# Optimization experiments

Hardware: AMD Instinct MI355X
Metric: run time of the kernel (lower is better)

The kernel has to match this reference:

```python
import jax, jax.numpy as jnp
import numpy as np

N_BLOCKS = 4
DIN = 4000      # features per input block
DE = 128        # embed dims per block
DLAT = 512      # latent dim per block
ALPHA = 0.3     # Keras LeakyReLU default negative slope


def setup_inputs() -> dict:
    key = jax.random.key(0)
    ks = jax.random.split(key, 7)
    N = 4096
    x = jax.random.normal(ks[0], (N, N_BLOCKS * DIN), dtype=jnp.float32)
    mask = jax.random.bernoulli(ks[1], 0.5, (N, N_BLOCKS * DIN))
    embed = jax.random.normal(ks[2], (N, N_BLOCKS * DE), dtype=jnp.float32)
    batches = jax.random.normal(ks[3], (N, 8), dtype=jnp.float32)
    mean_vals = jax.random.normal(ks[4], (N_BLOCKS * DIN,), dtype=jnp.float32)
    fan_in = DIN + DE + 8
    W = jax.random.normal(ks[5], (N_BLOCKS, fan_in, DLAT), dtype=jnp.float32) / np.sqrt(fan_in)
    b = jnp.zeros((N_BLOCKS, DLAT), dtype=jnp.float32)
    return {"x": x, "mask": mask, "embed": embed, "batches": batches,
            "mean_vals": mean_vals, "W": W, "b": b}


def reference(x, mask, embed, batches, mean_vals, W, b):
    N = x.shape[0]
    db = batches.shape[1]
    # masked mean-centering: x = where(mask, x - mean, 0)
    xm = jnp.where(mask, x - mean_vals[None, :], jnp.zeros((), x.dtype))
    # equal-sized splits == reshape into [N, B, din] / [N, B, de]
    xb = xm.reshape(N, N_BLOCKS, DIN)
    eb = embed.reshape(N, N_BLOCKS, DE)
    bb = jnp.broadcast_to(batches[:, None, :], (N, N_BLOCKS, db))
    inp = jnp.concatenate([xb, eb, bb], axis=-1)  # [N, B, DIN+DE+db]
    h = jnp.einsum('nbi,bio->nbo', inp, W) + b[None, :, :]  # grouped GEMM
    h = jnp.where(h >= 0, h, ALPHA * h)  # LeakyReLU(alpha=0.3)
    return h.reshape(N, N_BLOCKS * DLAT)  # concat of per-block outputs
```

## Files before the change

kernel.cpp:

```cpp
#include <hip/hip_runtime.h>

#define NROWS 4096
#define NBLK 4
#define DIN 4000
#define DE 128
#define DB 8
#define DLAT 512
#define FANIN 4136
#define KPAD 4224
#define NKT 66
#define XC 16000
#define OUTC 2048
#define TC 192

typedef __attribute__((ext_vector_type(8))) short short8;
typedef __attribute__((ext_vector_type(4))) float floatx4;

__device__ __forceinline__ unsigned short f2bf(float f) {
    unsigned int u = __builtin_bit_cast(unsigned int, f);
    u = (u + 0x7FFFu + ((u >> 16) & 1u)) >> 16;
    return (unsigned short)u;
}

__device__ __forceinline__ void async16(const void* g, void* l) {
    __builtin_amdgcn_global_load_lds(
        (const __attribute__((address_space(1))) void*)g,
        (__attribute__((address_space(3))) void*)l, 16, 0, 0);
}

__global__ void prep_w(const float* __restrict__ W, unsigned short* __restrict__ Wp) {
    __shared__ unsigned short tile[64 * 68];
    int bid = blockIdx.x;
    int nt = bid & 7;
    int t2 = bid >> 3;
    int kt = t2 % 66;
    int b  = t2 / 66;
    int tid = threadIdx.x;
    int n0 = nt * 64;
    int k0 = kt * 64;
#pragma unroll
    for (int i = 0; i < 4; ++i) {
        int c = i * 256 + tid;
        int r = c >> 4;
        int q = (c & 15) * 4;
        int pk = k0 + r;
        int wr = (pk < DIN) ? pk : ((pk >= 4032 && pk < 4168) ? pk - 32 : -1);
        float4 v = make_float4(0.f, 0.f, 0.f, 0.f);
        if (wr >= 0)
            v = *reinterpret_cast<const float4*>(W + ((size_t)b * FANIN + wr) * DLAT + n0 + q);
        ushort4 u4 = make_ushort4(f2bf(v.x), f2bf(v.y), f2bf(v.z), f2bf(v.w));
        *reinterpret_cast<ushort4*>(&tile[r * 68 + q]) = u4;
    }
    __syncthreads();
#pragma unroll
    for (int i = 0; i < 2; ++i) {
        int c = i * 256 + tid;
        int nl = c >> 3;
        int kc = c & 7;
        unsigned short o[8];
#pragma unroll
        for (int j = 0; j < 8; ++j) o[j] = tile[(kc * 8 + j) * 68 + nl];
        *reinterpret_cast<short8*>(Wp + ((size_t)(b * DLAT + n0 + nl)) * KPAD + k0 + kc * 8) =
            *reinterpret_cast<const short8*>(o);
    }
}

__global__ void prep_x(const float* __restrict__ x, const int* __restrict__ mask,
                       const float* __restrict__ mean, const float* __restrict__ embed,
                       const float* __restrict__ batches, unsigned short* __restrict__ Xp) {
    int c = blockIdx.x * 256 + threadIdx.x;
    int chunk = c % 528;
    int rb    = c / 528;
    int b   = rb & 3;
    int row = rb >> 2;
    int k   = chunk * 8;
    short8 v8 = (short8){0, 0, 0, 0, 0, 0, 0, 0};
    if (k < DIN) {
        size_t gi = (size_t)row * XC + b * DIN + k;
        const float4* xp = reinterpret_cast<const float4*>(x + gi);
        const int4*   mp = reinterpret_cast<const int4*>(mask + gi);
        const float4* ep = reinterpret_cast<const float4*>(mean + b * DIN + k);
        float4 x0 = xp[0], x1 = xp[1];
        int4   m0 = mp[0], m1 = mp[1];
        float4 e0 = ep[0], e1 = ep[1];
        float f0 = m0.x ? x0.x - e0.x : 0.f;
        float f1 = m0.y ? x0.y - e0.y : 0.f;
        float f2 = m0.z ? x0.z - e0.z : 0.f;
        float f3 = m0.w ? x0.w - e0.w : 0.f;
        float f4 = m1.x ? x1.x - e1.x : 0.f;
        float f5 = m1.y ? x1.y - e1.y : 0.f;
        float f6 = m1.z ? x1.z - e1.z : 0.f;
        float f7 = m1.w ? x1.w - e1.w : 0.f;
        v8 = (short8){(short)f2bf(f0), (short)f2bf(f1), (short)f2bf(f2), (short)f2bf(f3),
                      (short)f2bf(f4), (short)f2bf(f5), (short)f2bf(f6), (short)f2bf(f7)};
    } else if (k >= 4032 && k < 4160) {
        const float4* ep = reinterpret_cast<const float4*>(
            embed + (size_t)row * (NBLK * DE) + b * DE + (k - 4032));
        float4 a = ep[0], bb = ep[1];
        v8 = (short8){(short)f2bf(a.x), (short)f2bf(a.y), (short)f2bf(a.z), (short)f2bf(a.w),
                      (short)f2bf(bb.x), (short)f2bf(bb.y), (short)f2bf(bb.z), (short)f2bf(bb.w)};
    } else if (k == 4160) {
        const float4* bp = reinterpret_cast<const float4*>(batches + (size_t)row * DB);
        float4 a = bp[0], bb = bp[1];
        v8 = (short8){(short)f2bf(a.x), (short)f2bf(a.y), (short)f2bf(a.z), (short)f2bf(a.w),
                      (short)f2bf(bb.x), (short)f2bf(bb.y), (short)f2bf(bb.z), (short)f2bf(bb.w)};
    }
    *reinterpret_cast<short8*>(Xp + (size_t)rb * KPAD + k) = v8;
}

__global__ __launch_bounds__(256, 3) void gemm_x(
    const float* __restrict__ bias, const unsigned short* __restrict__ Wp,
    const unsigned short* __restrict__ Xp, float* __restrict__ out) {
    __shared__ unsigned short Asm_[128 * 64];
    __shared__ unsigned short Bsm_[128 * 64];

    int bid = blockIdx.x;
    int nt  = bid & 3;
    int b   = (bid >> 2) & 3;
    int mt  = bid >> 4;
    int tid  = threadIdx.x;
    int lane = tid & 63;
    int w    = tid >> 6;
    int wm   = w >> 1;
    int wn   = w & 1;
    int quad = lane >> 4;
    int l16  = lane & 15;
    int row0 = mt * 128;
    int n0   = nt * 128;

    floatx4 acc[4][4];
#pragma unroll
    for (int m = 0; m < 4; ++m)
#pragma unroll
        for (int n = 0; n < 4; ++n) acc[m][n] = (floatx4){0.f, 0.f, 0.f, 0.f};

    const unsigned short* Abase = Xp + ((size_t)row0 * NBLK + b) * KPAD;
    const unsigned short* Bbase = Wp + ((size_t)(b * DLAT + n0)) * KPAD;

    for (int kt = 0; kt < NKT; ++kt) {
        int k0 = kt * 64;
#pragma unroll
        for (int i = 0; i < 4; ++i) {
            int c  = i * 256 + tid;
            int r  = c >> 3;
            int cg = (c & 7) ^ (r & 7);
            async16(Abase + (size_t)r * (NBLK * KPAD) + k0 + cg * 8, &Asm_[c * 8]);
        }
#pragma unroll
        for (int i = 0; i < 4; ++i) {
            int c  = i * 256 + tid;
            int nl = c >> 3;
            int cg = (c & 7) ^ (nl & 7);
            async16(Bbase + (size_t)nl * KPAD + k0 + cg * 8, &Bsm_[c * 8]);
        }
        __syncthreads();
#pragma unroll
        for (int s = 0; s < 2; ++s) {
            short8 af[4], bfr[4];
#pragma unroll
            for (int m = 0; m < 4; ++m) {
                int ar = wm * 64 + m * 16 + l16;
                af[m] = *reinterpret_cast<const short8*>(
                    &Asm_[ar * 64 + (((s * 4 + quad) ^ (ar & 7)) * 8)]);
            }
#pragma unroll
            for (int n = 0; n < 4; ++n) {
                int br = wn * 64 + n * 16 + l16;
                bfr[n] = *reinterpret_cast<const short8*>(
                    &Bsm_[br * 64 + (((s * 4 + quad) ^ (br & 7)) * 8)]);
            }
#pragma unroll
            for (int m = 0; m < 4; ++m)
#pragma unroll
                for (int n = 0; n < 4; ++n)
                    acc[m][n] = __builtin_amdgcn_mfma_f32_16x16x32_bf16(
                        af[m], bfr[n], acc[m][n], 0, 0, 0);
        }
        __syncthreads();
    }

#pragma unroll
    for (int m = 0; m < 4; ++m) {
#pragma unroll
        for (int n = 0; n < 4; ++n) {
            int col_l = wn * 64 + n * 16 + l16;
            float bv = bias[b * DLAT + n0 + col_l];
#pragma unroll
            for (int r = 0; r < 4; ++r) {
                int row_l = wm * 64 + m * 16 + quad * 4 + r;
                float v = acc[m][n][r] + bv;
                v = v >= 0.f ? v : 0.3f * v;
                out[(size_t)(row0 + row_l) * OUTC + b * DLAT + n0 + col_l] = v;
            }
        }
    }
}

__global__ void prep_t(const float* __restrict__ embed, const float* __restrict__ batches,
                       unsigned short* __restrict__ T) {
    int i  = blockIdx.x * 256 + threadIdx.x;
    int t  = i % TC;
    int nb = i / TC;
    int b  = nb & 3;
    int n  = nb >> 2;
    float v = 0.f;
    if (t < DE)            v = embed[(size_t)n * (NBLK * DE) + b * DE + t];
    else if (t < DE + DB)  v = batches[(size_t)n * DB + (t - DE)];
    T[i] = f2bf(v);
}

__global__ __launch_bounds__(256, 3) void gemm_k(
    const float* __restrict__ x, const int* __restrict__ mask,
    const float* __restrict__ mean, const float* __restrict__ bias,
    const unsigned short* __restrict__ Wp, const unsigned short* __restrict__ T,
    float* __restrict__ out) {
    __shared__ unsigned short Asm_[128 * 64];
    __shared__ unsigned short Bsm_[128 * 64];

    int bid = blockIdx.x;
    int nt  = bid & 3;
    int b   = (bid >> 2) & 3;
    int mt  = bid >> 4;
    int tid  = threadIdx.x;
    int lane = tid & 63;
    int w    = tid >> 6;
    int wm   = w >> 1;
    int wn   = w & 1;
    int quad = lane >> 4;
    int l16  = lane & 15;
    int row0 = mt * 128;
    int n0   = nt * 128;

    floatx4 acc[4][4];
#pragma unroll
    for (int m = 0; m < 4; ++m)
#pragma unroll
        for (int n = 0; n < 4; ++n) acc[m][n] = (floatx4){0.f, 0.f, 0.f, 0.f};

    for (int kt = 0; kt < NKT; ++kt) {
        if (kt < 63) {
#pragma unroll
            for (int i = 0; i < 4; ++i) {
                int c  = i * 256 + tid;
                int r  = c >> 3;
                int cg = c & 7;
                int col = kt * 64 + cg * 8;
                short8 v8 = (short8){0, 0, 0, 0, 0, 0, 0, 0};
                if (col < DIN) {
                    size_t gi = (size_t)(row0 + r) * XC + (size_t)b * DIN + col;
                    const float4* xp = reinterpret_cast<const float4*>(x + gi);
                    const int4*   mp = reinterpret_cast<const int4*>(mask + gi);
                    const float4* ep = reinterpret_cast<const float4*>(mean + b * DIN + col);
                    float4 x0 = xp[0], x1 = xp[1];
                    int4   m0 = mp[0], m1 = mp[1];
                    float4 e0 = ep[0], e1 = ep[1];
                    float f0 = m0.x ? x0.x - e0.x : 0.f;
                    float f1 = m0.y ? x0.y - e0.y : 0.f;
                    float f2 = m0.z ? x0.z - e0.z : 0.f;
                    float f3 = m0.w ? x0.w - e0.w : 0.f;
                    float f4 = m1.x ? x1.x - e1.x : 0.f;
                    float f5 = m1.y ? x1.y - e1.y : 0.f;
                    float f6 = m1.z ? x1.z - e1.z : 0.f;
                    float f7 = m1.w ? x1.w - e1.w : 0.f;
                    v8 = (short8){(short)f2bf(f0), (short)f2bf(f1), (short)f2bf(f2),
                                  (short)f2bf(f3), (short)f2bf(f4), (short)f2bf(f5),
                                  (short)f2bf(f6), (short)f2bf(f7)};
                }
                *reinterpret_cast<short8*>(&Asm_[r * 64 + ((cg ^ (r & 7)) * 8)]) = v8;
            }
        } else {
#pragma unroll
            for (int i = 0; i < 4; ++i) {
                int c  = i * 256 + tid;
                int r  = c >> 3;
                int cg = (c & 7) ^ (r & 7);
                async16(T + ((size_t)(row0 + r) * NBLK + b) * TC + (kt - 63) * 64 + cg * 8,
                        &Asm_[c * 8]);
            }
        }
#pragma unroll
        for (int i = 0; i < 4; ++i) {
            int c  = i * 256 + tid;
            int nl = c >> 3;
            int cg = (c & 7) ^ (nl & 7);
            async16(Wp + ((size_t)(b * DLAT + n0 + nl)) * KPAD + kt * 64 + cg * 8,
                    &Bsm_[c * 8]);
        }
        __syncthreads();
#pragma unroll
        for (int s = 0; s < 2; ++s) {
            short8 af[4], bfr[4];
#pragma unroll
            for (int m = 0; m < 4; ++m) {
                int ar = wm * 64 + m * 16 + l16;
                af[m] = *reinterpret_cast<const short8*>(
                    &Asm_[ar * 64 + (((s * 4 + quad) ^ (ar & 7)) * 8)]);
            }
#pragma unroll
            for (int n = 0; n < 4; ++n) {
                int br = wn * 64 + n * 16 + l16;
                bfr[n] = *reinterpret_cast<const short8*>(
                    &Bsm_[br * 64 + (((s * 4 + quad) ^ (br & 7)) * 8)]);
            }
#pragma unroll
            for (int m = 0; m < 4; ++m)
#pragma unroll
                for (int n = 0; n < 4; ++n)
                    acc[m][n] = __builtin_amdgcn_mfma_f32_16x16x32_bf16(
                        af[m], bfr[n], acc[m][n], 0, 0, 0);
        }
        __syncthreads();
    }

#pragma unroll
    for (int m = 0; m < 4; ++m) {
#pragma unroll
        for (int n = 0; n < 4; ++n) {
            int col_l = wn * 64 + n * 16 + l16;
            float bv = bias[b * DLAT + n0 + col_l];
#pragma unroll
            for (int r = 0; r < 4; ++r) {
                int row_l = wm * 64 + m * 16 + quad * 4 + r;
                float v = acc[m][n][r] + bv;
                v = v >= 0.f ? v : 0.3f * v;
                out[(size_t)(row0 + row_l) * OUTC + b * DLAT + n0 + col_l] = v;
            }
        }
    }
}

extern "C" void kernel_launch(void* const* d_in, const int* in_sizes, int n_in,
                              void* d_out, int out_size, void* d_ws, size_t ws_size,
                              hipStream_t stream) {
    const float* x       = (const float*)d_in[0];
    const int*   mask    = (const int*)d_in[1];
    const float* embed   = (const float*)d_in[2];
    const float* batches = (const float*)d_in[3];
    const float* mean    = (const float*)d_in[4];
    const float* W       = (const float*)d_in[5];
    const float* bias    = (const float*)d_in[6];
    float* out = (float*)d_out;

    unsigned short* Wp = (unsigned short*)d_ws;
    size_t wp_elems = (size_t)NBLK * DLAT * KPAD;
    size_t xp_elems = (size_t)NROWS * NBLK * KPAD;
    size_t need_fast = (wp_elems + xp_elems) * 2;

    prep_w<<<dim3(2112), dim3(256), 0, stream>>>(W, Wp);

    if (ws_size >= need_fast) {
        unsigned short* Xp = Wp + wp_elems;
        prep_x<<<dim3(33792), dim3(256), 0, stream>>>(x, mask, mean, embed, batches, Xp);
        gemm_x<<<dim3(512), dim3(256), 0, stream>>>(bias, Wp, Xp, out);
    } else {
        unsigned short* T = Wp + wp_elems;
        prep_t<<<dim3(12288), dim3(256), 0, stream>>>(embed, batches, T);
        gemm_k<<<dim3(512), dim3(256), 0, stream>>>(x, mask, mean, bias, Wp, T, out);
    }
}
```

Before: 649.5 us.

## Fuse masked input preparation into a double-buffered grouped GEMM kernel

Drops the separate prep_x pass that wrote a bf16 copy of the centered inputs to workspace. The new gemm_f kernel reads x, mask, mean, embed and batches directly, applies the mask and mean subtraction, converts to bf16 in registers and writes the result to LDS. Global loads for the next k-tile are prefetched into registers and asynchronous LDS copies while the current tile runs on the MFMA units, using double-buffered LDS. Each block now covers 64 rows by the full 512 outputs of one block group with 512 threads. This removes a large intermediate write and re-read, but uses about 144KB of LDS per block, so only one block fits per CU and latency hiding rests on the prefetch.

```diff
diff --git a/kernel.cpp b/kernel.cpp
--- a/kernel.cpp
+++ b/kernel.cpp
@@ -13,8 +13,12 @@
 #define OUTC 2048
 #define TC 192
 
+#define PW_GRID 2112
+
 typedef __attribute__((ext_vector_type(8))) short short8;
 typedef __attribute__((ext_vector_type(4))) float floatx4;
+typedef float __attribute__((ext_vector_type(4))) f32x4;
+typedef int   __attribute__((ext_vector_type(4))) i32x4;
 
 __device__ __forceinline__ unsigned short f2bf(float f) {
     unsigned int u = __builtin_bit_cast(unsigned int, f);
@@ -65,68 +69,27 @@
     }
 }
 
-__global__ void prep_x(const float* __restrict__ x, const int* __restrict__ mask,
-                       const float* __restrict__ mean, const float* __restrict__ embed,
-                       const float* __restrict__ batches, unsigned short* __restrict__ Xp) {
-    int c = blockIdx.x * 256 + threadIdx.x;
-    int chunk = c % 528;
-    int rb    = c / 528;
-    int b   = rb & 3;
-    int row = rb >> 2;
-    int k   = chunk * 8;
-    short8 v8 = (short8){0, 0, 0, 0, 0, 0, 0, 0};
-    if (k < DIN) {
-        size_t gi = (size_t)row * XC + b * DIN + k;
-        const float4* xp = reinterpret_cast<const float4*>(x + gi);
-        const int4*   mp = reinterpret_cast<const int4*>(mask + gi);
-        const float4* ep = reinterpret_cast<const float4*>(mean + b * DIN + k);
-        float4 x0 = xp[0], x1 = xp[1];
-        int4   m0 = mp[0], m1 = mp[1];
-        float4 e0 = ep[0], e1 = ep[1];
-        float f0 = m0.x ? x0.x - e0.x : 0.f;
-        float f1 = m0.y ? x0.y - e0.y : 0.f;
-        float f2 = m0.z ? x0.z - e0.z : 0.f;
-        float f3 = m0.w ? x0.w - e0.w : 0.f;
-        float f4 = m1.x ? x1.x - e1.x : 0.f;
-        float f5 = m1.y ? x1.y - e1.y : 0.f;
-        float f6 = m1.z ? x1.z - e1.z : 0.f;
-        float f7 = m1.w ? x1.w - e1.w : 0.f;
-        v8 = (short8){(short)f2bf(f0), (short)f2bf(f1), (short)f2bf(f2), (short)f2bf(f3),
-                      (short)f2bf(f4), (short)f2bf(f5), (short)f2bf(f6), (short)f2bf(f7)};
-    } else if (k >= 4032 && k < 4160) {
-        const float4* ep = reinterpret_cast<const float4*>(
-            embed + (size_t)row * (NBLK * DE) + b * DE + (k - 4032));
-        float4 a = ep[0], bb = ep[1];
-        v8 = (short8){(short)f2bf(a.x), (short)f2bf(a.y), (short)f2bf(a.z), (short)f2bf(a.w),
-                      (short)f2bf(bb.x), (short)f2bf(bb.y), (short)f2bf(bb.z), (short)f2bf(bb.w)};
-    } else if (k == 4160) {
-        const float4* bp = reinterpret_cast<const float4*>(batches + (size_t)row * DB);
-        float4 a = bp[0], bb = bp[1];
-        v8 = (short8){(short)f2bf(a.x), (short)f2bf(a.y), (short)f2bf(a.z), (short)f2bf(a.w),
-                      (short)f2bf(bb.x), (short)f2bf(bb.y), (short)f2bf(bb.z), (short)f2bf(bb.w)};
-    }
-    *reinterpret_cast<short8*>(Xp + (size_t)rb * KPAD + k) = v8;
-}
-
-__global__ __launch_bounds__(256, 3) void gemm_x(
-    const float* __restrict__ bias, const unsigned short* __restrict__ Wp,
-    const unsigned short* __restrict__ Xp, float* __restrict__ out) {
-    __shared__ unsigned short Asm_[128 * 64];
-    __shared__ unsigned short Bsm_[128 * 64];
+__global__ __launch_bounds__(512, 2) void gemm_f(
+    const float* __restrict__ x, const int* __restrict__ mask,
+    const float* __restrict__ mean, const float* __restrict__ embed,
+    const float* __restrict__ batches, const float* __restrict__ bias,
+    const unsigned short* __restrict__ Wp, float* __restrict__ out) {
+    __shared__ unsigned short Asm_[2][64 * 64];
+    __shared__ unsigned short Bsm_[2][512 * 64];
 
     int bid = blockIdx.x;
-    int nt  = bid & 3;
-    int b   = (bid >> 2) & 3;
-    int mt  = bid >> 4;
+    int b   = bid & 3;
+    int mt  = bid >> 2;
+    int row0 = mt * 64;
     int tid  = threadIdx.x;
     int lane = tid & 63;
     int w    = tid >> 6;
-    int wm   = w >> 1;
-    int wn   = w & 1;
     int quad = lane >> 4;
     int l16  = lane & 15;
-    int row0 = mt * 128;
-    int n0   = nt * 128;
+    int r    = tid >> 3;
+    int cgl  = tid & 7;
+
+    const unsigned short* Bbase = Wp + (size_t)b * DLAT * KPAD;
 
     floatx4 acc[4][4];
 #pragma unroll
@@ -134,66 +97,133 @@
 #pragma unroll
         for (int n = 0; n < 4; ++n) acc[m][n] = (floatx4){0.f, 0.f, 0.f, 0.f};
 
-    const unsigned short* Abase = Xp + ((size_t)row0 * NBLK + b) * KPAD;
-    const unsigned short* Bbase = Wp + ((size_t)(b * DLAT + n0)) * KPAD;
-
+    f32x4 xa, xb, ea, eb;
+    i32x4 mka, mkb;
+    int amode;
+
+#define STAGE_B(NB, KT) do {                                                   \
+    int k0_ = (KT) * 64;                                                       \
+    _Pragma("unroll")                                                          \
+    for (int i_ = 0; i_ < 8; ++i_) {                                           \
+        int c_  = i_ * 512 + tid;                                              \
+        int nl_ = c_ >> 3;                                                     \
+        int cg_ = (c_ & 7) ^ (nl_ & 7);                                        \
+        async16(Bbase + (size_t)nl_ * KPAD + k0_ + cg_ * 8,                    \
+                &Bsm_[NB][c_ * 8]);                                            \
+    }                                                                          \
+} while (0)
+
+#define LOAD_A(KT) do {                                                        \
+    int col_ = (KT) * 64 + cgl * 8;                                            \
+    amode = 3;                                                                 \
+    if (col_ < DIN) {                                                          \
+        amode = 0;                                                             \
+        size_t gi_ = (size_t)(row0 + r) * XC + (size_t)b * DIN + col_;         \
+        const f32x4* xp_ = reinterpret_cast<const f32x4*>(x + gi_);            \
+        const i32x4* mp_ = reinterpret_cast<const i32x4*>(mask + gi_);         \
+        xa  = __builtin_nontemporal_load(xp_);                                 \
+        xb  = __builtin_nontemporal_load(xp_ + 1);                             \
+        mka = __builtin_nontemporal_load(mp_);                                 \
+        mkb = __builtin_nontemporal_load(mp_ + 1);                             \
+        const f32x4* ep_ = reinterpret_cast<const f32x4*>(mean + b * DIN + col_); \
+        ea = ep_[0]; eb = ep_[1];                                              \
+    } else if (col_ >= 4032 && col_ < 4160) {                                  \
+        amode = 1;                                                             \
+        const f32x4* ep_ = reinterpret_cast<const f32x4*>(                     \
+            embed + (size_t)(row0 + r) * (NBLK * DE) + b * DE + (col_ - 4032)); \
+        ea = ep_[0]; eb = ep_[1];                                              \
+    } else if (col_ == 4160) {                                                 \
+        amode = 1;                                                             \
+        const f32x4* bp_ = reinterpret_cast<const f32x4*>(                     \
+            batches + (size_t)(row0 + r) * DB);                                \
+        ea = bp_[0]; eb = bp_[1];                                              \
+    }                                                                          \
+} while (0)
+
+#define WRITE_A(NB) do {                                                       \
+    short8 v8_ = (short8){0, 0, 0, 0, 0, 0, 0, 0};                             \
+    if (amode == 0) {                                                          \
+        float f0_ = mka.x ? xa.x - ea.x : 0.f;                                 \
+        float f1_ = mka.y ? xa.y - ea.y : 0.f;                                 \
+        float f2_ = mka.z ? xa.z - ea.z : 0.f;                                 \
+        float f3_ = mka.w ? xa.w - ea.w : 0.f;                                 \
+        float f4_ = mkb.x ? xb.x - eb.x : 0.f;                                 \
+        float f5_ = mkb.y ? xb.y - eb.y : 0.f;                                 \
+        float f6_ = mkb.z ? xb.z - eb.z : 0.f;                                 \
+        float f7_ = mkb.w ? xb.w - eb.w : 0.f;                                 \
+        v8_ = (short8){(short)f2bf(f0_), (short)f2bf(f1_), (short)f2bf(f2_),   \
+                       (short)f2bf(f3_), (short)f2bf(f4_), (short)f2bf(f5_),   \
+                       (short)f2bf(f6_), (short)f2bf(f7_)};                    \
+    } else if (amode == 1) {                                                   \
+        v8_ = (short8){(short)f2bf(ea.x), (short)f2bf(ea.y), (short)f2bf(ea.z),\
+                       (short)f2bf(ea.w), (short)f2bf(eb.x), (short)f2bf(eb.y),\
+                       (short)f2bf(eb.z), (short)f2bf(eb.w)};                  \
+    }                                                                          \
+    *reinterpret_cast<short8*>(&Asm_[NB][r * 64 + ((cgl ^ (r & 7)) * 8)]) = v8_; \
+} while (0)
+
+#define COMPUTE(BUF) do {                                                      \
+    _Pragma("unroll")                                                          \
+    for (int s_ = 0; s_ < 2; ++s_) {                                           \
+        short8 af_[4], bf_[4];                                                 \
+        _Pragma("unroll")                                                      \
+        for (int m_ = 0; m_ < 4; ++m_) {                                       \
+            int ar_ = m_ * 16 + l16;                                           \
+            af_[m_] = *reinterpret_cast<const short8*>(                        \
+                &Asm_[BUF][ar_ * 64 + (((s_ * 4 + quad) ^ (ar_ & 7)) * 8)]);   \
+        }                                                                      \
+        _Pragma("unroll")                                                      \
+        for (int n_ = 0; n_ < 4; ++n_) {                                       \
+            int br_ = w * 64 + n_ * 16 + l16;                                  \
+            bf_[n_] = *reinterpret_cast<const short8*>(                        \
+                &Bsm_[BUF][br_ * 64 + (((s_ * 4 + quad) ^ (br_ & 7)) * 8)]);   \
+        }                                                                      \
+        _Pragma("unroll")                                                      \
+        for (int m_ = 0; m_ < 4; ++m_)                                         \
+            _Pragma("unroll")                                                  \
+            for (int n_ = 0; n_ < 4; ++n_)                                     \
+                acc[m_][n_] = __builtin_amdgcn_mfma_f32_16x16x32_bf16(         \
+                    af_[m_], bf_[n_], acc[m_][n_], 0, 0, 0);                   \
+    }                                                                          \
+} while (0)
+
+    LOAD_A(0);
+    STAGE_B(0, 0);
+    WRITE_A(0);
+    __syncthreads();
+
+    int buf = 0;
     for (int kt = 0; kt < NKT; ++kt) {
-        int k0 = kt * 64;
-#pragma unroll
-        for (int i = 0; i < 4; ++i) {
-            int c  = i * 256 + tid;
-            int r  = c >> 3;
-            int cg = (c & 7) ^ (r & 7);
-            async16(Abase + (size_t)r * (NBLK * KPAD) + k0 + cg * 8, &Asm_[c * 8]);
-        }
-#pragma unroll
-        for (int i = 0; i < 4; ++i) {
-            int c  = i * 256 + tid;
-            int nl = c >> 3;
-            int cg = (c & 7) ^ (nl & 7);
-            async16(Bbase + (size_t)nl * KPAD + k0 + cg * 8, &Bsm_[c * 8]);
-        }
+        int nb = buf ^ 1;
+        if (kt + 1 < NKT) {
+            LOAD_A(kt + 1);
+            STAGE_B(nb, kt + 1);
+        }
+        COMPUTE(buf);
+        if (kt + 1 < NKT) WRITE_A(nb);
         __syncthreads();
-#pragma unroll
-        for (int s = 0; s < 2; ++s) {
-            short8 af[4], bfr[4];
-#pragma unroll
-            for (int m = 0; m < 4; ++m) {
-                int ar = wm * 64 + m * 16 + l16;
-                af[m] = *reinterpret_cast<const short8*>(
-                    &Asm_[ar * 64 + (((s * 4 + quad) ^ (ar & 7)) * 8)]);
-            }
-#pragma unroll
-            for (int n = 0; n < 4; ++n) {
-                int br = wn * 64 + n * 16 + l16;
-                bfr[n] = *reinterpret_cast<const short8*>(
-                    &Bsm_[br * 64 + (((s * 4 + quad) ^ (br & 7)) * 8)]);
-            }
-#pragma unroll
-            for (int m = 0; m < 4; ++m)
-#pragma unroll
-                for (int n = 0; n < 4; ++n)
-                    acc[m][n] = __builtin_amdgcn_mfma_f32_16x16x32_bf16(
-                        af[m], bfr[n], acc[m][n], 0, 0, 0);
-        }
-        __syncthreads();
+        buf = nb;
     }
 
 #pragma unroll
     for (int m = 0; m < 4; ++m) {
 #pragma unroll
         for (int n = 0; n < 4; ++n) {
-            int col_l = wn * 64 + n * 16 + l16;
-            float bv = bias[b * DLAT + n0 + col_l];
-#pragma unroll
-            for (int r = 0; r < 4; ++r) {
-                int row_l = wm * 64 + m * 16 + quad * 4 + r;
-                float v = acc[m][n][r] + bv;
+            int col_l = w * 64 + n * 16 + l16;
+            float bv = bias[b * DLAT + col_l];
+#pragma unroll
+            for (int rr = 0; rr < 4; ++rr) {
+                int row_l = m * 16 + quad * 4 + rr;
+                float v = acc[m][n][rr] + bv;
                 v = v >= 0.f ? v : 0.3f * v;
-                out[(size_t)(row0 + row_l) * OUTC + b * DLAT + n0 + col_l] = v;
-            }
-        }
-    }
+                out[(size_t)(row0 + row_l) * OUTC + b * DLAT + col_l] = v;
+            }
+        }
+    }
+#undef STAGE_B
+#undef LOAD_A
+#undef WRITE_A
+#undef COMPUTE
 }
 
 __global__ void prep_t(const float* __restrict__ embed, const float* __restrict__ batches,
@@ -343,15 +373,13 @@
 
     unsigned short* Wp = (unsigned short*)d_ws;
     size_t wp_elems = (size_t)NBLK * DLAT * KPAD;
-    size_t xp_elems = (size_t)NROWS * NBLK * KPAD;
-    size_t need_fast = (wp_elems + xp_elems) * 2;
-
-    prep_w<<<dim3(2112), dim3(256), 0, stream>>>(W, Wp);
-
-    if (ws_size >= need_fast) {
-        unsigned short* Xp = Wp + wp_elems;
-        prep_x<<<dim3(33792), dim3(256), 0, stream>>>(x, mask, mean, embed, batches, Xp);
-        gemm_x<<<dim3(512), dim3(256), 0, stream>>>(bias, Wp, Xp, out);
+    size_t wp_bytes = wp_elems * 2;
+
+    prep_w<<<dim3(PW_GRID), dim3(256), 0, stream>>>(W, Wp);
+
+    if (ws_size >= wp_bytes + (size_t)(NROWS * NBLK * TC) * 2) {
+        gemm_f<<<dim3(256), dim3(512), 0, stream>>>(
+            x, mask, mean, embed, batches, bias, Wp, out);
     } else {
         unsigned short* T = Wp + wp_elems;
         prep_t<<<dim3(12288), dim3(256), 0, stream>>>(embed, batches, T);
```

After: 613.3 us. -5.6%, faster.
